# Kernel optimization log

Measured on AMD Instinct MI355X. Metric: run time of the kernel, lower is better.

The kernel has to match this reference:

```python
import jax, jax.numpy as jnp
import numpy as np
import math

EMB_DIM = 1024
HEADS = 16
HEAD_DIM = EMB_DIM // HEADS
B, S = 2, 2048


def setup_inputs() -> dict:
    key = jax.random.key(0)
    k1, k2, k3, k4, k5 = jax.random.split(key, 5)
    X = jax.random.normal(k1, (B, S, EMB_DIM), dtype=jnp.float32)
    # causal mask: positions with 0.0 are masked to -inf (masked_fill(mask == 0.0, -inf))
    mask = jnp.tril(jnp.ones((S, S), dtype=jnp.float32))
    scale = 1.0 / math.sqrt(EMB_DIM)
    # torch Linear(emb_dim, 3*emb_dim): y = x @ W.T + b; store W pre-transposed [E, 3E]
    W_qkv = jax.random.normal(k2, (EMB_DIM, 3 * EMB_DIM), dtype=jnp.float32) * scale
    b_qkv = jnp.zeros((3 * EMB_DIM,), dtype=jnp.float32)
    W_o = jax.random.normal(k3, (EMB_DIM, EMB_DIM), dtype=jnp.float32) * scale
    b_o = jnp.zeros((EMB_DIM,), dtype=jnp.float32)
    return {"X": X, "mask": mask, "W_qkv": W_qkv, "b_qkv": b_qkv, "W_o": W_o, "b_o": b_o}


def reference(X, mask, W_qkv, b_qkv, W_o, b_o):
    # X: [B, S, E]
    Bn, Sn, E = X.shape
    qkv = X @ W_qkv + b_qkv                                   # [B, S, 3E]
    qkv = qkv.reshape(Bn, Sn, 3, HEADS, HEAD_DIM)
    qkv = jnp.transpose(qkv, (2, 0, 3, 1, 4))                  # [3, B, H, S, d]
    Q, K, V = qkv[0], qkv[1], qkv[2]
    inv_sqrt_d = 1.0 / math.sqrt(HEAD_DIM)
    scores = jnp.einsum('bhqd,bhkd->bhqk', Q, K) * inv_sqrt_d  # [B, H, S, S]
    scores = jnp.where(mask == 0.0, -jnp.inf, scores)
    attn = jax.nn.softmax(scores, axis=-1)
    # dropout omitted (eval mode / deterministic reference)
    out = jnp.einsum('bhqk,bhkd->bhqd', attn, V)               # [B, H, S, d]
    out = jnp.transpose(out, (0, 2, 1, 3)).reshape(Bn, Sn, E)
    return out @ W_o + b_o
```

## Files before the change

kernel.cpp:

```cpp
#include <hip/hip_runtime.h>
#include <hip/hip_bf16.h>
#include <cstdint>
#include <cstddef>

typedef __bf16 bf16_t;
typedef __attribute__((ext_vector_type(8))) __bf16 bf16x8;
typedef __attribute__((ext_vector_type(4))) __bf16 bf16x4;
typedef __attribute__((ext_vector_type(4))) float f32x4;

#define AS1 __attribute__((address_space(1)))
#define AS3 __attribute__((address_space(3)))

static constexpr int Bn = 2, Sn = 2048, En = 1024, Hn = 16, Dn = 64;

__device__ __forceinline__ uint32_t cvt_pk_bf16(float lo, float hi) {
  uint32_t r;
  asm("v_cvt_pk_bf16_f32 %0, %1, %2" : "=v"(r) : "v"(lo), "v"(hi));
  return r;
}

__global__ __launch_bounds__(256) void convert_f32_bf16(
    const float* __restrict__ in, bf16_t* __restrict__ out, int n) {
  int i = (blockIdx.x * 256 + threadIdx.x) * 4;
  if (i < n) {
    float4 v = *(const float4*)(in + i);
    bf16x4 o;
    o[0] = (bf16_t)v.x; o[1] = (bf16_t)v.y; o[2] = (bf16_t)v.z; o[3] = (bf16_t)v.w;
    *(bf16x4*)(out + i) = o;
  }
}

__global__ __launch_bounds__(256) void transpose_conv(
    const float* __restrict__ in, bf16_t* __restrict__ out, int R, int C) {
  __shared__ float tile[32][33];
  int bx = blockIdx.x * 32, by = blockIdx.y * 32;
  int tx = threadIdx.x & 31, ty = threadIdx.x >> 5;
#pragma unroll
  for (int i = 0; i < 32; i += 8)
    tile[ty + i][tx] = in[(size_t)(by + ty + i) * C + bx + tx];
  __syncthreads();
#pragma unroll
  for (int i = 0; i < 32; i += 8)
    out[(size_t)(bx + ty + i) * R + by + tx] = (bf16_t)tile[tx][ty + i];
}

__global__ __launch_bounds__(256) void transpose_v(
    const bf16_t* __restrict__ V, bf16_t* __restrict__ Vt) {
  __shared__ ushort tile[64][65];
  int bh = blockIdx.y, s0 = blockIdx.x * 64;
  int t = threadIdx.x;
  const ushort* src = (const ushort*)(V + ((size_t)bh * Sn + s0) * 64);
#pragma unroll
  for (int p = 0; p < 4; ++p) {
    int s = p * 16 + (t >> 4);
    int c = (t & 15) * 4;
    ushort4 v = *(const ushort4*)(src + (size_t)s * 64 + c);
    tile[s][c] = v.x; tile[s][c + 1] = v.y; tile[s][c + 2] = v.z; tile[s][c + 3] = v.w;
  }
  __syncthreads();
  ushort* dst = (ushort*)(Vt + ((size_t)bh * 64) * Sn + s0);
#pragma unroll
  for (int p = 0; p < 4; ++p) {
    int d = p * 16 + (t >> 4);
    int c = (t & 15) * 4;
    ushort4 v;
    v.x = tile[c][d]; v.y = tile[c + 1][d]; v.z = tile[c + 2][d]; v.w = tile[c + 3][d];
    *(ushort4*)(dst + (size_t)d * Sn + c) = v;
  }
}

template <int K_, int BM>
__device__ __forceinline__ void gemm_core(
    const bf16_t* __restrict__ A, const bf16_t* __restrict__ Bt,
    f32x4 (&acc)[BM / 32][4], int& col0, int& row0) {
  __shared__ bf16_t As[2][BM * 32];
  __shared__ bf16_t Bs[2][128 * 32];
  const int tid = threadIdx.x, lane = tid & 63, wid = tid >> 6;
  const int wm = wid >> 1, wn = wid & 1;
  const int m0 = blockIdx.y * BM, n0 = blockIdx.x * 128;
  const int KT = K_ / 32;
  constexpr int MI = BM / 32;

  auto stage = [&](bf16_t* as, bf16_t* bs, int kt) {
    int csw = ((lane & 3) ^ ((lane >> 2) & 3)) * 8;
#pragma unroll
    for (int j = 0; j < BM / 64; ++j) {
      int r0 = wid * (BM / 4) + j * 16;
      const bf16_t* ga = A + (size_t)(m0 + r0 + (lane >> 2)) * K_ + kt * 32 + csw;
      __builtin_amdgcn_global_load_lds((const AS1 void*)ga, (AS3 void*)(as + r0 * 32), 16, 0, 0);
    }
#pragma unroll
    for (int j = 0; j < 2; ++j) {
      int r0 = wid * 32 + j * 16;
      const bf16_t* gb = Bt + (size_t)(n0 + r0 + (lane >> 2)) * K_ + kt * 32 + csw;
      __builtin_amdgcn_global_load_lds((const AS1 void*)gb, (AS3 void*)(bs + r0 * 32), 16, 0, 0);
    }
  };
  auto compute = [&](const bf16_t* as, const bf16_t* bs) {
    bf16x8 af[MI], bfr[4];
    uint32_t swz = (uint32_t)(((lane >> 4) ^ (lane & 3)) << 4);
#pragma unroll
    for (int mi = 0; mi < MI; ++mi) {
      uint32_t row = (uint32_t)(wm * (BM / 2) + mi * 16 + (lane & 15));
      af[mi] = *(const bf16x8*)((const char*)as + row * 64 + swz);
    }
#pragma unroll
    for (int ni = 0; ni < 4; ++ni) {
      uint32_t row = (uint32_t)(wn * 64 + ni * 16 + (lane & 15));
      bfr[ni] = *(const bf16x8*)((const char*)bs + row * 64 + swz);
    }
#pragma unroll
    for (int mi = 0; mi < MI; ++mi)
#pragma unroll
      for (int ni = 0; ni < 4; ++ni)
        acc[mi][ni] = __builtin_amdgcn_mfma_f32_16x16x32_bf16(af[mi], bfr[ni], acc[mi][ni], 0, 0, 0);
  };

  stage(As[0], Bs[0], 0);
  __syncthreads();
  int cur = 0;
  for (int kt = 0; kt < KT - 1; ++kt) {
    stage(As[cur ^ 1], Bs[cur ^ 1], kt + 1);
    compute(As[cur], Bs[cur]);
    __syncthreads();
    cur ^= 1;
  }
  compute(As[cur], Bs[cur]);
  col0 = n0 + wn * 64 + (lane & 15);
  row0 = m0 + wm * (BM / 2) + ((lane >> 4) << 2);
}

__global__ __launch_bounds__(256) void gemm_qkv(
    const bf16_t* __restrict__ A, const bf16_t* __restrict__ Bt,
    const float* __restrict__ bias, bf16_t* __restrict__ Qb,
    bf16_t* __restrict__ Kb, bf16_t* __restrict__ Vb) {
  f32x4 acc[4][4] = {};
  int col0, row0;
  gemm_core<1024, 128>(A, Bt, acc, col0, row0);
#pragma unroll
  for (int ni = 0; ni < 4; ++ni) {
    int n = col0 + ni * 16;
    float bv = bias[n];
    int which = n >> 10, nn = n & 1023;
    int h = nn >> 6, dd = nn & 63;
    bf16_t* dst = which == 0 ? Qb : (which == 1 ? Kb : Vb);
    float scl = which == 0 ? 0.125f * 1.44269504f : 1.0f;
#pragma unroll
    for (int mi = 0; mi < 4; ++mi)
#pragma unroll
      for (int i = 0; i < 4; ++i) {
        int m = row0 + mi * 16 + i;
        int b = m >> 11, s = m & 2047;
        float v = (acc[mi][ni][i] + bv) * scl;
        dst[(((size_t)b * Hn + h) * Sn + s) * 64 + dd] = (bf16_t)v;
      }
  }
}

__global__ __launch_bounds__(256) void gemm_out(
    const bf16_t* __restrict__ A, const bf16_t* __restrict__ Bt,
    const float* __restrict__ bias, float* __restrict__ out) {
  f32x4 acc[2][4] = {};
  int col0, row0;
  gemm_core<1024, 64>(A, Bt, acc, col0, row0);
#pragma unroll
  for (int ni = 0; ni < 4; ++ni) {
    int n = col0 + ni * 16;
    float bv = bias[n];
#pragma unroll
    for (int mi = 0; mi < 2; ++mi)
#pragma unroll
      for (int i = 0; i < 4; ++i) {
        int m = row0 + mi * 16 + i;
        out[(size_t)m * En + n] = acc[mi][ni][i] + bv;
      }
  }
}

__global__ __launch_bounds__(256) void attn_fwd(
    const bf16_t* __restrict__ Qb, const bf16_t* __restrict__ Kb,
    const bf16_t* __restrict__ Vt, bf16_t* __restrict__ AO) {
  __shared__ bf16_t Ks[2][64 * 64];
  __shared__ bf16_t Vs[2][64 * 64];
  __shared__ bf16_t Ps[4][16 * 64];
  const int tid = threadIdx.x, lane = tid & 63, wid = tid >> 6;
  const int bh = blockIdx.x;
  const int y = blockIdx.y, gy = y & 7, ky = y >> 3;
  const int q_tile = ky == 0 ? 31 - gy : (ky == 1 ? 16 + gy : (ky == 2 ? 15 - gy : gy));
  const int nt = q_tile + 1;
  const int qb = q_tile * 64 + wid * 16;
  const int qmy = qb + (lane & 15);

  const int rl = lane >> 3;
  const int cp = lane & 7;
  auto issueKV = [&](int buf, int t) {
#pragma unroll
    for (int j = 0; j < 2; ++j) {
      int r = wid * 16 + j * 8 + rl;
      int sc = cp ^ rl;
      const bf16_t* gk = Kb + (((size_t)bh * Sn + t * 64 + r) << 6) + (sc << 3);
      __builtin_amdgcn_global_load_lds((const AS1 void*)gk,
          (AS3 void*)(&Ks[buf][wid * 1024 + j * 512]), 16, 0, 0);
      const bf16_t* gv = Vt + ((size_t)bh * 64 + r) * Sn + t * 64 + (sc << 3);
      __builtin_amdgcn_global_load_lds((const AS1 void*)gv,
          (AS3 void*)(&Vs[buf][wid * 1024 + j * 512]), 16, 0, 0);
    }
  };

  const int srcA = (((lane & 15) + ((lane & 16) << 1)) << 2);
  const int srcB = srcA + 64;
  const bool hi = lane >= 32;

  bf16x8 aq[2];
  {
    const bf16_t* qp = Qb + ((size_t)bh * Sn + qb + (lane & 15)) * 64 + ((lane >> 4) << 3);
    aq[0] = *(const bf16x8*)qp;
    aq[1] = *(const bf16x8*)(qp + 32);
  }
  f32x4 O[4] = {};
  float m_run = -1e30f, l_run = 0.f;

  int buf = 0;
  issueKV(0, 0);

  for (int t = 0; t < nt; ++t) {
    asm volatile("s_waitcnt vmcnt(0)" ::: "memory");
    __syncthreads();
    if (t + 1 < nt) issueKV(buf ^ 1, t + 1);
    const char* ksb = (const char*)Ks[buf];
    const char* vsb = (const char*)Vs[buf];
    f32x4 sc[4];
    __builtin_amdgcn_s_setprio(1);
#pragma unroll
    for (int ni = 0; ni < 4; ++ni) {
      int kvr = ni * 16 + (lane & 15);
      uint32_t o0 = (uint32_t)(kvr * 128 + ((lane >> 4) << 4)) ^ (uint32_t)((kvr & 7) << 4);
      uint32_t o1 = (uint32_t)(kvr * 128 + 64 + ((lane >> 4) << 4)) ^ (uint32_t)((kvr & 7) << 4);
      bf16x8 b0 = *(const bf16x8*)(ksb + o0);
      bf16x8 b1 = *(const bf16x8*)(ksb + o1);
      f32x4 z = {};
      z = __builtin_amdgcn_mfma_f32_16x16x32_bf16(b0, aq[0], z, 0, 0, 0);
      sc[ni] = __builtin_amdgcn_mfma_f32_16x16x32_bf16(b1, aq[1], z, 0, 0, 0);
    }
    __builtin_amdgcn_s_setprio(0);
    if (t == nt - 1) {
#pragma unroll
      for (int ni = 0; ni < 4; ++ni) {
        int kvbase = t * 64 + ni * 16 + ((lane >> 4) << 2);
#pragma unroll
        for (int i = 0; i < 4; ++i)
          if (kvbase + i > qmy) sc[ni][i] = -1e30f;
      }
    }
    float mt = sc[0][0];
#pragma unroll
    for (int ni = 0; ni < 4; ++ni)
#pragma unroll
      for (int i = 0; i < 4; ++i) mt = fmaxf(mt, sc[ni][i]);
    mt = fmaxf(mt, __shfl_xor(mt, 16));
    mt = fmaxf(mt, __shfl_xor(mt, 32));
    if (!__all(mt <= m_run + 11.5f)) {
      float mn = fmaxf(m_run, mt);
      float s = __builtin_exp2f(m_run - mn);
      m_run = mn;
      l_run *= s;
#pragma unroll
      for (int n2 = 0; n2 < 4; ++n2)
#pragma unroll
        for (int i = 0; i < 4; ++i) O[n2][i] *= s;
    }
    float rs = 0.f;
    uint32_t pk[4][2];
#pragma unroll
    for (int ni = 0; ni < 4; ++ni) {
      float p0 = __builtin_exp2f(sc[ni][0] - m_run);
      float p1 = __builtin_exp2f(sc[ni][1] - m_run);
      float p2 = __builtin_exp2f(sc[ni][2] - m_run);
      float p3 = __builtin_exp2f(sc[ni][3] - m_run);
      rs += (p0 + p1) + (p2 + p3);
      pk[ni][0] = cvt_pk_bf16(p0, p1);
      pk[ni][1] = cvt_pk_bf16(p2, p3);
    }
    rs += __shfl_xor(rs, 16);
    rs += __shfl_xor(rs, 32);
    l_run += rs;
    union U8 { uint32_t u[4]; bf16x8 v; } pw0, pw1;
#pragma unroll
    for (int w = 0; w < 4; ++w) {
      int srci = (w < 2) ? srcA : srcB;
      uint32_t x0 = (uint32_t)__builtin_amdgcn_ds_bpermute(srci, (int)pk[0][w & 1]);
      uint32_t y0 = (uint32_t)__builtin_amdgcn_ds_bpermute(srci, (int)pk[1][w & 1]);
      pw0.u[w] = hi ? y0 : x0;
      uint32_t x1 = (uint32_t)__builtin_amdgcn_ds_bpermute(srci, (int)pk[2][w & 1]);
      uint32_t y1 = (uint32_t)__builtin_amdgcn_ds_bpermute(srci, (int)pk[3][w & 1]);
      pw1.u[w] = hi ? y1 : x1;
    }
    __builtin_amdgcn_s_setprio(1);
#pragma unroll
    for (int n2 = 0; n2 < 4; ++n2) {
      int dr = n2 * 16 + (lane & 15);
      uint32_t o0 = (uint32_t)(dr * 128 + ((lane >> 4) << 4)) ^ (uint32_t)((dr & 7) << 4);
      uint32_t o1 = (uint32_t)(dr * 128 + 64 + ((lane >> 4) << 4)) ^ (uint32_t)((dr & 7) << 4);
      bf16x8 v0 = *(const bf16x8*)(vsb + o0);
      bf16x8 v1 = *(const bf16x8*)(vsb + o1);
      O[n2] = __builtin_amdgcn_mfma_f32_16x16x32_bf16(v0, pw0.v, O[n2], 0, 0, 0);
      O[n2] = __builtin_amdgcn_mfma_f32_16x16x32_bf16(v1, pw1.v, O[n2], 0, 0, 0);
    }
    __builtin_amdgcn_s_setprio(0);
    buf ^= 1;
  }
  char* pw = (char*)Ps[wid];
  const float inv = 1.0f / l_run;
  const int ql = lane & 15, g = lane >> 4;
#pragma unroll
  for (int n2 = 0; n2 < 4; ++n2)
#pragma unroll
    for (int p2 = 0; p2 < 2; ++p2) {
      uint32_t w = cvt_pk_bf16(O[n2][2 * p2] * inv, O[n2][2 * p2 + 1] * inv);
      uint32_t byte = (uint32_t)(ql * 128 + n2 * 32 + g * 8 + p2 * 4) ^ (uint32_t)((ql & 7) << 4);
      *(uint32_t*)(pw + byte) = w;
    }
  asm volatile("s_waitcnt lgkmcnt(0)" ::: "memory");
  __builtin_amdgcn_sched_barrier(0);
  int b = bh >> 4, h = bh & 15;
#pragma unroll
  for (int i = 0; i < 4; ++i) {
    int ql2 = (g << 2) + i;
    int qrow = qb + ql2;
#pragma unroll
    for (int n2 = 0; n2 < 4; ++n2) {
      int d = n2 * 16 + ql;
      uint32_t byte = (uint32_t)(ql2 * 128 + d * 2) ^ (uint32_t)((ql2 & 7) << 4);
      AO[((size_t)b * Sn + qrow) * En + h * 64 + d] = *(bf16_t*)(pw + byte);
    }
  }
}

extern "C" void kernel_launch(void* const* d_in, const int* in_sizes, int n_in,
                              void* d_out, int out_size, void* d_ws, size_t ws_size,
                              hipStream_t stream) {
  const float* X     = (const float*)d_in[0];
  const float* W_qkv = (const float*)d_in[2];
  const float* b_qkv = (const float*)d_in[3];
  const float* W_o   = (const float*)d_in[4];
  const float* b_o   = (const float*)d_in[5];
  float* out = (float*)d_out;

  char* ws = (char*)d_ws;
  bf16_t* Xb  = (bf16_t*)(ws);
  bf16_t* WqT = (bf16_t*)(ws + 8388608);
  bf16_t* WoT = (bf16_t*)(ws + 14680064);
  bf16_t* Qb  = (bf16_t*)(ws + 16777216);
  bf16_t* Kb  = (bf16_t*)(ws + 25165824);
  bf16_t* Vb  = (bf16_t*)(ws + 33554432);
  bf16_t* Vt  = (bf16_t*)(ws + 41943040);
  bf16_t* AO  = (bf16_t*)(ws + 50331648);

  convert_f32_bf16<<<4096, 256, 0, stream>>>(X, Xb, Bn * Sn * En);
  transpose_conv<<<dim3(96, 32), 256, 0, stream>>>(W_qkv, WqT, 1024, 3072);
  transpose_conv<<<dim3(32, 32), 256, 0, stream>>>(W_o, WoT, 1024, 1024);
  gemm_qkv<<<dim3(24, 32), 256, 0, stream>>>(Xb, WqT, b_qkv, Qb, Kb, Vb);
  transpose_v<<<dim3(32, 32), 256, 0, stream>>>(Vb, Vt);
  attn_fwd<<<dim3(32, 32), 256, 0, stream>>>(Qb, Kb, Vt, AO);
  gemm_out<<<dim3(8, 64), 256, 0, stream>>>(AO, WoT, b_o, out);
}
```

Measured before the change: 216.6 us.

## Split long causal query tiles across two KV halves with combine kernel

Query tiles in the upper half of the sequence have their KV loop split into two blocks, each writing unnormalized partial outputs plus running max and sum to workspace. A new combine kernel merges the two partials with log-sum-exp weighting into the attention output. A constant slot order schedules the heaviest work first. This shortens the longest per-block critical path and balances causal work across CUs, at the cost of an extra launch and bf16 partial round-trips through memory, which add rounding.

New measurement: 219.0 us. About the same (+1.1%).

```diff
diff --git a/kernel.cpp b/kernel.cpp
--- a/kernel.cpp
+++ b/kernel.cpp
@@ -18,6 +18,12 @@
   asm("v_cvt_pk_bf16_f32 %0, %1, %2" : "=v"(r) : "v"(lo), "v"(hi));
   return r;
 }
+
+__constant__ int kSlotOrder[48] = {
+  15, 31, 46, 47,  14, 29, 30, 44, 45,  13, 27, 28, 42, 43,
+  12, 25, 26, 40, 41,  11, 23, 24, 38, 39,  10, 21, 22, 36, 37,
+   9, 19, 20, 34, 35,   8, 17, 18, 32, 33,   7, 16,
+   6, 5, 4, 3, 2, 1, 0};
 
 __global__ __launch_bounds__(256) void convert_f32_bf16(
     const float* __restrict__ in, bf16_t* __restrict__ out, int n) {
@@ -179,15 +185,19 @@
 
 __global__ __launch_bounds__(256) void attn_fwd(
     const bf16_t* __restrict__ Qb, const bf16_t* __restrict__ Kb,
-    const bf16_t* __restrict__ Vt, bf16_t* __restrict__ AO) {
+    const bf16_t* __restrict__ Vt, bf16_t* __restrict__ AO,
+    bf16_t* __restrict__ Opart, float* __restrict__ ml) {
   __shared__ bf16_t Ks[2][64 * 64];
   __shared__ bf16_t Vs[2][64 * 64];
   __shared__ bf16_t Ps[4][16 * 64];
   const int tid = threadIdx.x, lane = tid & 63, wid = tid >> 6;
   const int bh = blockIdx.x;
-  const int y = blockIdx.y, gy = y & 7, ky = y >> 3;
-  const int q_tile = ky == 0 ? 31 - gy : (ky == 1 ? 16 + gy : (ky == 2 ? 15 - gy : gy));
-  const int nt = q_tile + 1;
+  const int s = kSlotOrder[blockIdx.y];
+  int q_tile, t0, t1, part;
+  if (s < 16)      { q_tile = s;      t0 = 0;                  t1 = s + 1;      part = 0; }
+  else if (s < 32) { q_tile = s;      t0 = 0;                  t1 = (s + 1) >> 1; part = 0; }
+  else             { q_tile = s - 16; t0 = (q_tile + 1) >> 1;  t1 = q_tile + 1; part = 1; }
+  const bool is_split = (s >= 16);
   const int qb = q_tile * 64 + wid * 16;
   const int qmy = qb + (lane & 15);
 
@@ -221,12 +231,12 @@
   float m_run = -1e30f, l_run = 0.f;
 
   int buf = 0;
-  issueKV(0, 0);
-
-  for (int t = 0; t < nt; ++t) {
+  issueKV(0, t0);
+
+  for (int t = t0; t < t1; ++t) {
     asm volatile("s_waitcnt vmcnt(0)" ::: "memory");
     __syncthreads();
-    if (t + 1 < nt) issueKV(buf ^ 1, t + 1);
+    if (t + 1 < t1) issueKV(buf ^ 1, t + 1);
     const char* ksb = (const char*)Ks[buf];
     const char* vsb = (const char*)Vs[buf];
     f32x4 sc[4];
@@ -243,7 +253,7 @@
       sc[ni] = __builtin_amdgcn_mfma_f32_16x16x32_bf16(b1, aq[1], z, 0, 0, 0);
     }
     __builtin_amdgcn_s_setprio(0);
-    if (t == nt - 1) {
+    if (t == q_tile) {
 #pragma unroll
       for (int ni = 0; ni < 4; ++ni) {
         int kvbase = t * 64 + ni * 16 + ((lane >> 4) << 2);
@@ -261,13 +271,13 @@
     mt = fmaxf(mt, __shfl_xor(mt, 32));
     if (!__all(mt <= m_run + 11.5f)) {
       float mn = fmaxf(m_run, mt);
-      float s = __builtin_exp2f(m_run - mn);
+      float sc2 = __builtin_exp2f(m_run - mn);
       m_run = mn;
-      l_run *= s;
+      l_run *= sc2;
 #pragma unroll
       for (int n2 = 0; n2 < 4; ++n2)
 #pragma unroll
-        for (int i = 0; i < 4; ++i) O[n2][i] *= s;
+        for (int i = 0; i < 4; ++i) O[n2][i] *= sc2;
     }
     float rs = 0.f;
     uint32_t pk[4][2];
@@ -309,9 +319,27 @@
     __builtin_amdgcn_s_setprio(0);
     buf ^= 1;
   }
+  const int ql = lane & 15, g = lane >> 4;
+  if (is_split) {
+    size_t pb = (((size_t)bh * 16 + (q_tile - 16)) << 1) + part;
+    bf16_t* ob = Opart + (pb << 12) + (size_t)(wid * 16 + ql) * 64;
+#pragma unroll
+    for (int n2 = 0; n2 < 4; ++n2) {
+      uint32_t w0 = cvt_pk_bf16(O[n2][0], O[n2][1]);
+      uint32_t w1 = cvt_pk_bf16(O[n2][2], O[n2][3]);
+      uint32_t* dst = (uint32_t*)(ob + n2 * 16 + g * 4);
+      dst[0] = w0;
+      dst[1] = w1;
+    }
+    if (g == 0) {
+      float* mlb = ml + (pb << 7);
+      mlb[wid * 16 + ql] = m_run;
+      mlb[64 + wid * 16 + ql] = l_run;
+    }
+    return;
+  }
   char* pw = (char*)Ps[wid];
   const float inv = 1.0f / l_run;
-  const int ql = lane & 15, g = lane >> 4;
 #pragma unroll
   for (int n2 = 0; n2 < 4; ++n2)
 #pragma unroll
@@ -334,6 +362,38 @@
       AO[((size_t)b * Sn + qrow) * En + h * 64 + d] = *(bf16_t*)(pw + byte);
     }
   }
+}
+
+__global__ __launch_bounds__(256) void attn_combine(
+    const bf16_t* __restrict__ Opart, const float* __restrict__ ml,
+    bf16_t* __restrict__ AO) {
+  const int qt16 = blockIdx.x, bh = blockIdx.y;
+  const int tid = threadIdx.x;
+  const int q = tid >> 2, dq = (tid & 3) << 4;
+  size_t pb = (((size_t)bh * 16 + qt16) << 1);
+  const float* ml0 = ml + (pb << 7);
+  const float* ml1 = ml + ((pb + 1) << 7);
+  float m0 = ml0[q], l0 = ml0[64 + q];
+  float m1 = ml1[q], l1 = ml1[64 + q];
+  float M = fmaxf(m0, m1);
+  float w0 = __builtin_exp2f(m0 - M), w1 = __builtin_exp2f(m1 - M);
+  float inv = 1.0f / (l0 * w0 + l1 * w1);
+  float f0 = w0 * inv, f1 = w1 * inv;
+  const bf16_t* o0 = Opart + (pb << 12) + (size_t)q * 64 + dq;
+  const bf16_t* o1 = Opart + ((pb + 1) << 12) + (size_t)q * 64 + dq;
+  bf16x8 a0 = *(const bf16x8*)o0, a0b = *(const bf16x8*)(o0 + 8);
+  bf16x8 a1 = *(const bf16x8*)o1, a1b = *(const bf16x8*)(o1 + 8);
+  bf16x8 r0, r1;
+#pragma unroll
+  for (int j = 0; j < 8; ++j) {
+    r0[j] = (bf16_t)(f0 * (float)a0[j] + f1 * (float)a1[j]);
+    r1[j] = (bf16_t)(f0 * (float)a0b[j] + f1 * (float)a1b[j]);
+  }
+  int b = bh >> 4, h = bh & 15;
+  int qrow = (16 + qt16) * 64 + q;
+  bf16_t* dst = AO + ((size_t)b * Sn + qrow) * En + h * 64 + dq;
+  *(bf16x8*)dst = r0;
+  *(bf16x8*)(dst + 8) = r1;
 }
 
 extern "C" void kernel_launch(void* const* d_in, const int* in_sizes, int n_in,
@@ -355,12 +415,15 @@
   bf16_t* Vb  = (bf16_t*)(ws + 33554432);
   bf16_t* Vt  = (bf16_t*)(ws + 41943040);
   bf16_t* AO  = (bf16_t*)(ws + 50331648);
+  bf16_t* Opart = (bf16_t*)(ws);
+  float*  Oml   = (float*)(ws + 8388608);
 
   convert_f32_bf16<<<4096, 256, 0, stream>>>(X, Xb, Bn * Sn * En);
   transpose_conv<<<dim3(96, 32), 256, 0, stream>>>(W_qkv, WqT, 1024, 3072);
   transpose_conv<<<dim3(32, 32), 256, 0, stream>>>(W_o, WoT, 1024, 1024);
   gemm_qkv<<<dim3(24, 32), 256, 0, stream>>>(Xb, WqT, b_qkv, Qb, Kb, Vb);
   transpose_v<<<dim3(32, 32), 256, 0, stream>>>(Vb, Vt);
-  attn_fwd<<<dim3(32, 32), 256, 0, stream>>>(Qb, Kb, Vt, AO);
+  attn_fwd<<<dim3(32, 48), 256, 0, stream>>>(Qb, Kb, Vt, AO, Opart, Oml);
+  attn_combine<<<dim3(16, 32), 256, 0, stream>>>(Opart, Oml, AO);
   gemm_out<<<dim3(8, 64), 256, 0, stream>>>(AO, WoT, b_o, out);
 }
```
